# Optimization experiments

Hardware: AMD Instinct MI355X
Metric: run time of the kernel (lower is better)

Reference implementation:

```python
import jax, jax.numpy as jnp
import numpy as np

Q_DIM, KV_DIM, N_HEAD, C, OUT_DIM, N_AXIS = 256, 256, 8, 32, 256, 1
B, S = 1, 2048

def setup_inputs() -> dict:
    key = jax.random.key(0)
    ks = jax.random.split(key, 9)
    sd = 0.05
    return {
        "q_inputs": jax.random.normal(ks[0], (B, S, Q_DIM), jnp.float32),
        "kv_inputs": jax.random.normal(ks[1], (B, S, KV_DIM), jnp.float32),
        "bias": jax.random.normal(ks[2], (B, N_HEAD, S, S), jnp.float32),
        "qg_weights": jax.random.normal(ks[3], (Q_DIM, N_AXIS, N_HEAD, 2 * C), jnp.float32) * sd,
        "kv_weights": jax.random.normal(ks[4], (KV_DIM, N_AXIS, N_HEAD, 2 * C), jnp.float32) * sd,
        "qg_bias": jax.random.normal(ks[5], (N_AXIS, N_HEAD, 1, 2 * C), jnp.float32) * sd,
        "kv_bias": jax.random.normal(ks[6], (N_AXIS, N_HEAD, 1, 2 * C), jnp.float32) * sd,
        "o_weights": jax.random.normal(ks[7], (N_AXIS, N_HEAD, C, OUT_DIM), jnp.float32) * sd,
        "o_bias": jax.random.normal(ks[8], (OUT_DIM, N_AXIS), jnp.float32) * sd,
    }

def reference(q_inputs, kv_inputs, bias, qg_weights, kv_weights, qg_bias, kv_bias, o_weights, o_bias):
    scale = C ** (-0.5)
    # to_unsqueeze path: add axis dim r (=n_axis=1)
    qi = q_inputs[..., None]          # (B, q, q_dim, r)
    ki = kv_inputs[..., None]         # (B, k, kv_dim, r)
    b = bias[:, None]                 # (B, 1, h, q, k) broadcasts over r
    # per-axis, per-head QKV projections with bias
    qg = jnp.einsum('bqar,arhc->brhqc', qi, qg_weights) + qg_bias
    q, g = jnp.split(qg, 2, axis=-1)  # (B, r, h, q, c) each
    kv = jnp.einsum('bkar,arhc->brhkc', ki, kv_weights) + kv_bias
    k, v = jnp.split(kv, 2, axis=-1)  # (B, r, h, k, c) each
    logits = jnp.einsum('brhqc,brhkc->brhqk', q * scale, k) + b
    attn = jax.nn.softmax(logits, axis=-1)
    attn_out = jnp.einsum('brhqk,brhkc->brhqc', attn, v)
    attn_out = attn_out * jax.nn.sigmoid(g)  # gating
    output = jnp.einsum('brhqc,rhco->bqor', attn_out, o_weights) + o_bias
    return output[..., 0]  # squeeze the n_axis dim (to_unsqueeze path)
```

## Files before the change

kernel.cpp:

```cpp
#include <hip/hip_runtime.h>
#include <hip/hip_bf16.h>
#include <math.h>

#define SEQ   2048
#define NHEAD 8

typedef __attribute__((ext_vector_type(8))) short bf16x8;
typedef __attribute__((ext_vector_type(4))) short bf16x4;
typedef __attribute__((ext_vector_type(4))) float f32x4;

static __device__ __forceinline__ short f2bf(float f) {
    __hip_bfloat16 h = __float2bfloat16(f);
    return *reinterpret_cast<short*>(&h);
}

__global__ __launch_bounds__(256)
void prep_w_kernel(const float* __restrict__ qg_w, const float* __restrict__ kv_w,
                   const float* __restrict__ o_w, short* __restrict__ wqgT,
                   short* __restrict__ wkvT, short* __restrict__ owT)
{
    __shared__ float t[64][65];
    int bid = blockIdx.x;
    const float* src; short* dst; int N, tr, tc;
    if (bid < 32)      { src = qg_w; dst = wqgT; N = 512; tr = bid >> 3; tc = bid & 7; }
    else if (bid < 64) { bid -= 32; src = kv_w; dst = wkvT; N = 512; tr = bid >> 3; tc = bid & 7; }
    else               { bid -= 64; src = o_w;  dst = owT;  N = 256; tr = bid >> 2; tc = bid & 3; }

    const int tid = threadIdx.x;
    const int rr = tid >> 6;
    const int cc = tid & 63;
#pragma unroll
    for (int s = 0; s < 16; s++)
        t[(s << 2) + rr][cc] =
            src[(size_t)((tr << 6) + (s << 2) + rr) * N + (tc << 6) + cc];
    __syncthreads();
#pragma unroll
    for (int s = 0; s < 16; s++)
        dst[(size_t)((tc << 6) + (s << 2) + rr) * 256 + (tr << 6) + cc]
            = f2bf(t[cc][(s << 2) + rr]);
}

__global__ __launch_bounds__(256, 4)
void proj_qgkv_kernel(const float* __restrict__ q_in, const float* __restrict__ kv_in,
                      const short* __restrict__ wqgT, const short* __restrict__ wkvT,
                      const float* __restrict__ qg_b, const float* __restrict__ kv_b,
                      short* __restrict__ qs, float* __restrict__ gs,
                      short* __restrict__ ks, short* __restrict__ vP)
{
    const int z = blockIdx.z;
    const float* __restrict__ A  = z ? kv_in : q_in;
    const short* __restrict__ W  = z ? wkvT : wqgT;
    const float* __restrict__ bv = z ? kv_b : qg_b;

    const int tid = threadIdx.x;
    const int wq = tid >> 6, lane = tid & 63;
    const int ln = lane & 15, quad = lane >> 4;
    const int m0 = blockIdx.x << 6;
    const int n0 = blockIdx.y << 5;

    f32x4 acc[2];
#pragma unroll
    for (int nt = 0; nt < 2; nt++) {
        const float b = bv[n0 + (nt << 4) + ln];
        acc[nt] = (f32x4){b, b, b, b};
    }

    const float* ap = A + (size_t)(m0 + (wq << 4) + ln) * 256 + (quad << 3);
    const short* wp = W + (size_t)(n0 + ln) * 256 + (quad << 3);

    float4 a4[2][2]; bf16x8 wb[2][2];
    auto ldp = [&](int b, int k8) {
        a4[b][0] = *(const float4*)(ap + (k8 << 5));
        a4[b][1] = *(const float4*)(ap + (k8 << 5) + 4);
        wb[b][0] = *(const bf16x8*)(wp + (k8 << 5));
        wb[b][1] = *(const bf16x8*)(wp + 4096 + (k8 << 5));
    };
    ldp(0, 0);
#pragma unroll
    for (int k8 = 0; k8 < 8; k8++) {
        const int b = k8 & 1;
        if (k8 < 7) ldp(b ^ 1, k8 + 1);
        bf16x8 a;
        a[0] = f2bf(a4[b][0].x); a[1] = f2bf(a4[b][0].y);
        a[2] = f2bf(a4[b][0].z); a[3] = f2bf(a4[b][0].w);
        a[4] = f2bf(a4[b][1].x); a[5] = f2bf(a4[b][1].y);
        a[6] = f2bf(a4[b][1].z); a[7] = f2bf(a4[b][1].w);
        acc[0] = __builtin_amdgcn_mfma_f32_16x16x32_bf16(a, wb[b][0], acc[0], 0, 0, 0);
        acc[1] = __builtin_amdgcn_mfma_f32_16x16x32_bf16(a, wb[b][1], acc[1], 0, 0, 0);
    }

    const float scale = 0.17677669529663689f;
#pragma unroll
    for (int nt = 0; nt < 2; nt++) {
        const int n = n0 + (nt << 4) + ln;
        const int h = n >> 6, c2 = n & 63;
        if (z == 0) {
#pragma unroll
            for (int r = 0; r < 4; r++) {
                const int m = m0 + (wq << 4) + (quad << 2) + r;
                const float v = acc[nt][r];
                if (c2 < 32) qs[(((h << 11) + m) << 5) + c2] = f2bf(v * scale);
                else gs[(((h << 11) + m) << 5) + (c2 - 32)] = 1.0f / (1.0f + __expf(-v));
            }
        } else if (c2 < 32) {
#pragma unroll
            for (int r = 0; r < 4; r++) {
                const int m = m0 + (wq << 4) + (quad << 2) + r;
                ks[(((h << 11) + m) << 5) + c2] = f2bf(acc[nt][r]);
            }
        } else {
            const int c  = c2 - 32;
            const int kt = m0 >> 6;
            const int kc = wq >> 1;
            const int jb = (wq & 1) << 2;
            bf16x4 v4;
            v4[0] = f2bf(acc[nt][0]); v4[1] = f2bf(acc[nt][1]);
            v4[2] = f2bf(acc[nt][2]); v4[3] = f2bf(acc[nt][3]);
            *(bf16x4*)(vP + (size_t)((((h << 5) + kt) * 2 + kc) * 4 + quad) * 256
                          + (c << 3) + jb) = v4;
        }
    }
}

template<int NTILE>
__global__ __launch_bounds__(256, 3)
void attn_kernel(const short* __restrict__ qs, const short* __restrict__ ks,
                 const short* __restrict__ vP, const float* __restrict__ bias,
                 float* __restrict__ Opart, float* __restrict__ mpart,
                 float* __restrict__ lpart)
{
    const int h = blockIdx.y, z = blockIdx.z;
    const int q0 = blockIdx.x << 6;
    const int tid = threadIdx.x;
    const int wq = tid >> 6, lane = tid & 63;
    const int ln = lane & 15, quad = lane >> 4;

    const int qrow = q0 + (wq << 4) + ln;
    const bf16x8 qf = *(const bf16x8*)(qs + (((size_t)(h << 11) + qrow) << 5) + (quad << 3));

    const float L2E = 1.44269504088896f;
    float ml2 = -1e30f, l = 0.f;
    f32x4 O0 = {0, 0, 0, 0}, O1 = {0, 0, 0, 0};

    const int kbeg = z * (NTILE << 6);
    const float* bp  = bias + ((size_t)h * SEQ + qrow) * SEQ + kbeg + (quad << 2);
    const short* kp  = ks + (((size_t)(h << 11) + kbeg + ln) << 5) + (quad << 3);
    const short* vp0 = vP + (size_t)((((h << 5) + (kbeg >> 6)) * 2) * 4 + quad) * 256
                          + (ln << 3);

    f32x4 cb[2][4]; bf16x8 kf[2][4]; bf16x8 vf[2][2][2];
    auto ld = [&](int b, int t) {
#pragma unroll
        for (int mt = 0; mt < 4; mt++) {
            cb[b][mt] = *(const f32x4*)(bp + (t << 6) + (mt << 4));
            kf[b][mt] = *(const bf16x8*)(kp + ((size_t)((t << 6) + (mt << 4)) << 5));
        }
#pragma unroll
        for (int kc = 0; kc < 2; kc++)
#pragma unroll
            for (int cm = 0; cm < 2; cm++)
                vf[b][cm][kc] = *(const bf16x8*)(vp0 + (size_t)(t << 11)
                                                 + (kc << 10) + (cm << 7));
    };

    ld(0, 0);
#pragma unroll
    for (int kt = 0; kt < NTILE; kt++) {
        const int b = kt & 1;
        if (kt + 1 < NTILE) ld(b ^ 1, kt + 1);

        f32x4 S[4];
#pragma unroll
        for (int mt = 0; mt < 4; mt++)
            S[mt] = __builtin_amdgcn_mfma_f32_16x16x32_bf16(kf[b][mt], qf,
                                                            cb[b][mt], 0, 0, 0);

        float smax = S[0][0];
#pragma unroll
        for (int mt = 0; mt < 4; mt++)
#pragma unroll
            for (int r = 0; r < 4; r++) smax = fmaxf(smax, S[mt][r]);
        smax = fmaxf(smax, __shfl_xor(smax, 16));
        smax = fmaxf(smax, __shfl_xor(smax, 32));
        const float mnew = fmaxf(ml2, smax * L2E);
        const float alpha = exp2f(ml2 - mnew);
        ml2 = mnew;

        float pr[4][4];
        float rs = 0.f;
#pragma unroll
        for (int mt = 0; mt < 4; mt++)
#pragma unroll
            for (int r = 0; r < 4; r++) {
                const float p = exp2f(fmaf(S[mt][r], L2E, -mnew));
                pr[mt][r] = p;
                rs += p;
            }
        rs += __shfl_xor(rs, 16);
        rs += __shfl_xor(rs, 32);
        l = l * alpha + rs;

        short pb[4][4];
#pragma unroll
        for (int mt = 0; mt < 4; mt++)
#pragma unroll
            for (int r = 0; r < 4; r++) pb[mt][r] = f2bf(pr[mt][r]);
        bf16x8 P0 = {pb[0][0], pb[0][1], pb[0][2], pb[0][3],
                     pb[1][0], pb[1][1], pb[1][2], pb[1][3]};
        bf16x8 P1 = {pb[2][0], pb[2][1], pb[2][2], pb[2][3],
                     pb[3][0], pb[3][1], pb[3][2], pb[3][3]};

        O0 *= alpha;
        O1 *= alpha;
        O0 = __builtin_amdgcn_mfma_f32_16x16x32_bf16(vf[b][0][0], P0, O0, 0, 0, 0);
        O1 = __builtin_amdgcn_mfma_f32_16x16x32_bf16(vf[b][1][0], P0, O1, 0, 0, 0);
        O0 = __builtin_amdgcn_mfma_f32_16x16x32_bf16(vf[b][0][1], P1, O0, 0, 0, 0);
        O1 = __builtin_amdgcn_mfma_f32_16x16x32_bf16(vf[b][1][1], P1, O1, 0, 0, 0);
    }

    const size_t pb_ = (((size_t)(z * NHEAD + h)) << 11) + qrow;
    if (quad == 0) { mpart[pb_] = ml2; lpart[pb_] = l; }
    float* op = Opart + (pb_ << 5);
    *(f32x4*)(op + (quad << 2))      = O0;
    *(f32x4*)(op + 16 + (quad << 2)) = O1;
}

__global__ __launch_bounds__(256)
void combine_kernel(const float* __restrict__ Opart, const float* __restrict__ mpart,
                    const float* __restrict__ lpart, const float* __restrict__ gs,
                    short* __restrict__ att, int nsplit)
{
    const int g  = blockIdx.x * 256 + threadIdx.x;
    const int c4 = g & 7;
    const int q  = (g >> 3) & (SEQ - 1);
    const int h  = g >> 14;

    float M = -1e30f;
    for (int s = 0; s < nsplit; s++)
        M = fmaxf(M, mpart[(((size_t)s * NHEAD + h) << 11) + q]);

    float l = 0.f;
    float4 O = {0.f, 0.f, 0.f, 0.f};
    for (int s = 0; s < nsplit; s++) {
        const size_t base = (((size_t)s * NHEAD + h) << 11) + q;
        const float w = exp2f(mpart[base] - M);
        l += w * lpart[base];
        float4 o4 = *(const float4*)(Opart + (base << 5) + (c4 << 2));
        O.x = fmaf(w, o4.x, O.x); O.y = fmaf(w, o4.y, O.y);
        O.z = fmaf(w, o4.z, O.z); O.w = fmaf(w, o4.w, O.w);
    }
    const float inv = 1.0f / l;
    float4 g4 = *(const float4*)(gs + ((((size_t)h << 11) + q) << 5) + (c4 << 2));
    bf16x4 r;
    r[0] = f2bf(O.x * inv * g4.x); r[1] = f2bf(O.y * inv * g4.y);
    r[2] = f2bf(O.z * inv * g4.z); r[3] = f2bf(O.w * inv * g4.w);
    *(bf16x4*)(att + ((size_t)q << 8) + (h << 5) + (c4 << 2)) = r;
}

__global__ __launch_bounds__(256, 4)
void proj_o_kernel(const short* __restrict__ att, const short* __restrict__ owT,
                   const float* __restrict__ o_b, float* __restrict__ out)
{
    const int tid = threadIdx.x;
    const int wq = tid >> 6, lane = tid & 63;
    const int ln = lane & 15, quad = lane >> 4;
    const int m0 = blockIdx.x << 6;
    const int n0 = blockIdx.y << 4;

    const int n = n0 + ln;
    const float b = o_b[n];
    f32x4 acc = (f32x4){b, b, b, b};

    const short* ap = att + (size_t)(m0 + (wq << 4) + ln) * 256 + (quad << 3);
    const short* bp = owT + (size_t)n * 256 + (quad << 3);

    bf16x8 a2[2], w2[2];
    a2[0] = *(const bf16x8*)(ap);  w2[0] = *(const bf16x8*)(bp);
#pragma unroll
    for (int k8 = 0; k8 < 8; k8++) {
        const int b_ = k8 & 1;
        if (k8 < 7) {
            a2[b_ ^ 1] = *(const bf16x8*)(ap + ((k8 + 1) << 5));
            w2[b_ ^ 1] = *(const bf16x8*)(bp + ((k8 + 1) << 5));
        }
        acc = __builtin_amdgcn_mfma_f32_16x16x32_bf16(a2[b_], w2[b_], acc, 0, 0, 0);
    }
#pragma unroll
    for (int r = 0; r < 4; r++) {
        const int m = m0 + (wq << 4) + (quad << 2) + r;
        out[(size_t)m * 256 + n] = acc[r];
    }
}

extern "C" void kernel_launch(void* const* d_in, const int* in_sizes, int n_in,
                              void* d_out, int out_size, void* d_ws, size_t ws_size,
                              hipStream_t stream)
{
    const float* q_in  = (const float*)d_in[0];
    const float* kv_in = (const float*)d_in[1];
    const float* bias  = (const float*)d_in[2];
    const float* qg_w  = (const float*)d_in[3];
    const float* kv_w  = (const float*)d_in[4];
    const float* qg_b  = (const float*)d_in[5];
    const float* kv_b  = (const float*)d_in[6];
    const float* o_w   = (const float*)d_in[7];
    const float* o_b   = (const float*)d_in[8];
    float* out = (float*)d_out;

    char* p = (char*)d_ws;
    short* qs   = (short*)p; p += 1048576;
    short* ksb  = (short*)p; p += 1048576;
    short* vPb  = (short*)p; p += 1048576;
    short* attb = (short*)p; p += 1048576;
    short* wqgT = (short*)p; p += 262144;
    short* wkvT = (short*)p; p += 262144;
    short* owT  = (short*)p; p += 131072;
    float* gs   = (float*)p; p += 2097152;

    const size_t fixed = (size_t)(p - (char*)d_ws);
    int nsplit = 1;
    {
        const int cand[4] = {8, 4, 2, 1};
        for (int i = 0; i < 4; i++) {
            size_t ns = (size_t)cand[i];
            if (fixed + ns * (size_t)(2097152 + 2 * 65536) <= ws_size) {
                nsplit = cand[i]; break;
            }
        }
    }
    float* mp = (float*)p;
    float* lp = mp + (size_t)nsplit * NHEAD * SEQ;
    float* Op = lp + (size_t)nsplit * NHEAD * SEQ;

    hipLaunchKernelGGL(prep_w_kernel, dim3(80), dim3(256), 0, stream,
                       qg_w, kv_w, o_w, wqgT, wkvT, owT);
    hipLaunchKernelGGL(proj_qgkv_kernel, dim3(32, 16, 2), dim3(256), 0, stream,
                       q_in, kv_in, wqgT, wkvT, qg_b, kv_b, qs, gs, ksb, vPb);
    switch (nsplit) {
    case 8:
        hipLaunchKernelGGL((attn_kernel<4>), dim3(32, NHEAD, 8), dim3(256), 0, stream,
                           qs, ksb, vPb, bias, Op, mp, lp); break;
    case 4:
        hipLaunchKernelGGL((attn_kernel<8>), dim3(32, NHEAD, 4), dim3(256), 0, stream,
                           qs, ksb, vPb, bias, Op, mp, lp); break;
    case 2:
        hipLaunchKernelGGL((attn_kernel<16>), dim3(32, NHEAD, 2), dim3(256), 0, stream,
                           qs, ksb, vPb, bias, Op, mp, lp); break;
    default:
        hipLaunchKernelGGL((attn_kernel<32>), dim3(32, NHEAD, 1), dim3(256), 0, stream,
                           qs, ksb, vPb, bias, Op, mp, lp); break;
    }
    hipLaunchKernelGGL(combine_kernel, dim3(512), dim3(256), 0, stream,
                       Op, mp, lp, gs, attb, nsplit);
    hipLaunchKernelGGL(proj_o_kernel, dim3(32, 16), dim3(256), 0, stream,
                       attb, owT, o_b, out);
}
```

Baseline: 248.5 us.

## Raise attention occupancy, shrink V prefetch, and drop split-8 path

Attention now targets four blocks per SIMD instead of three. V fragments are loaded at the start of each tile instead of being double-buffered, and the probability buffer reuses the S registers, all to lower register pressure. The key-sequence split drops from 8 to at most 4, so each block handles 8 tiles, which halves the partial buffers the combine step reads. The cost is V load latency exposed inside each iteration and fewer blocks in the grid.

```diff
diff --git a/kernel.cpp b/kernel.cpp
--- a/kernel.cpp
+++ b/kernel.cpp
@@ -123,7 +123,7 @@
 }
 
 template<int NTILE>
-__global__ __launch_bounds__(256, 3)
+__global__ __launch_bounds__(256, 4)
 void attn_kernel(const short* __restrict__ qs, const short* __restrict__ ks,
                  const short* __restrict__ vP, const float* __restrict__ bias,
                  float* __restrict__ Opart, float* __restrict__ mpart,
@@ -148,26 +148,28 @@
     const short* vp0 = vP + (size_t)((((h << 5) + (kbeg >> 6)) * 2) * 4 + quad) * 256
                           + (ln << 3);
 
-    f32x4 cb[2][4]; bf16x8 kf[2][4]; bf16x8 vf[2][2][2];
-    auto ld = [&](int b, int t) {
+    f32x4 cb[2][4]; bf16x8 kf[2][4];
+    auto ld_cbkf = [&](int b, int t) {
 #pragma unroll
         for (int mt = 0; mt < 4; mt++) {
             cb[b][mt] = *(const f32x4*)(bp + (t << 6) + (mt << 4));
             kf[b][mt] = *(const bf16x8*)(kp + ((size_t)((t << 6) + (mt << 4)) << 5));
         }
-#pragma unroll
-        for (int kc = 0; kc < 2; kc++)
-#pragma unroll
-            for (int cm = 0; cm < 2; cm++)
-                vf[b][cm][kc] = *(const bf16x8*)(vp0 + (size_t)(t << 11)
-                                                 + (kc << 10) + (cm << 7));
     };
 
-    ld(0, 0);
+    ld_cbkf(0, 0);
 #pragma unroll
     for (int kt = 0; kt < NTILE; kt++) {
         const int b = kt & 1;
-        if (kt + 1 < NTILE) ld(b ^ 1, kt + 1);
+
+        bf16x8 vf[2][2];
+#pragma unroll
+        for (int kc = 0; kc < 2; kc++)
+#pragma unroll
+            for (int cm = 0; cm < 2; cm++)
+                vf[cm][kc] = *(const bf16x8*)(vp0 + (size_t)(kt << 11)
+                                              + (kc << 10) + (cm << 7));
+        if (kt + 1 < NTILE) ld_cbkf(b ^ 1, kt + 1);
 
         f32x4 S[4];
 #pragma unroll
@@ -186,36 +188,34 @@
         const float alpha = exp2f(ml2 - mnew);
         ml2 = mnew;
 
-        float pr[4][4];
         float rs = 0.f;
 #pragma unroll
         for (int mt = 0; mt < 4; mt++)
 #pragma unroll
             for (int r = 0; r < 4; r++) {
                 const float p = exp2f(fmaf(S[mt][r], L2E, -mnew));
-                pr[mt][r] = p;
+                S[mt][r] = p;
                 rs += p;
             }
         rs += __shfl_xor(rs, 16);
         rs += __shfl_xor(rs, 32);
         l = l * alpha + rs;
 
-        short pb[4][4];
-#pragma unroll
-        for (int mt = 0; mt < 4; mt++)
-#pragma unroll
-            for (int r = 0; r < 4; r++) pb[mt][r] = f2bf(pr[mt][r]);
-        bf16x8 P0 = {pb[0][0], pb[0][1], pb[0][2], pb[0][3],
-                     pb[1][0], pb[1][1], pb[1][2], pb[1][3]};
-        bf16x8 P1 = {pb[2][0], pb[2][1], pb[2][2], pb[2][3],
-                     pb[3][0], pb[3][1], pb[3][2], pb[3][3]};
+        bf16x8 P0, P1;
+#pragma unroll
+        for (int r = 0; r < 4; r++) {
+            P0[r]     = f2bf(S[0][r]);
+            P0[4 + r] = f2bf(S[1][r]);
+            P1[r]     = f2bf(S[2][r]);
+            P1[4 + r] = f2bf(S[3][r]);
+        }
 
         O0 *= alpha;
         O1 *= alpha;
-        O0 = __builtin_amdgcn_mfma_f32_16x16x32_bf16(vf[b][0][0], P0, O0, 0, 0, 0);
-        O1 = __builtin_amdgcn_mfma_f32_16x16x32_bf16(vf[b][1][0], P0, O1, 0, 0, 0);
-        O0 = __builtin_amdgcn_mfma_f32_16x16x32_bf16(vf[b][0][1], P1, O0, 0, 0, 0);
-        O1 = __builtin_amdgcn_mfma_f32_16x16x32_bf16(vf[b][1][1], P1, O1, 0, 0, 0);
+        O0 = __builtin_amdgcn_mfma_f32_16x16x32_bf16(vf[0][0], P0, O0, 0, 0, 0);
+        O1 = __builtin_amdgcn_mfma_f32_16x16x32_bf16(vf[1][0], P0, O1, 0, 0, 0);
+        O0 = __builtin_amdgcn_mfma_f32_16x16x32_bf16(vf[0][1], P1, O0, 0, 0, 0);
+        O1 = __builtin_amdgcn_mfma_f32_16x16x32_bf16(vf[1][1], P1, O1, 0, 0, 0);
     }
 
     const size_t pb_ = (((size_t)(z * NHEAD + h)) << 11) + qrow;
@@ -320,8 +320,8 @@
     const size_t fixed = (size_t)(p - (char*)d_ws);
     int nsplit = 1;
     {
-        const int cand[4] = {8, 4, 2, 1};
-        for (int i = 0; i < 4; i++) {
+        const int cand[3] = {4, 2, 1};
+        for (int i = 0; i < 3; i++) {
             size_t ns = (size_t)cand[i];
             if (fixed + ns * (size_t)(2097152 + 2 * 65536) <= ws_size) {
                 nsplit = cand[i]; break;
@@ -337,9 +337,6 @@
     hipLaunchKernelGGL(proj_qgkv_kernel, dim3(32, 16, 2), dim3(256), 0, stream,
                        q_in, kv_in, wqgT, wkvT, qg_b, kv_b, qs, gs, ksb, vPb);
     switch (nsplit) {
-    case 8:
-        hipLaunchKernelGGL((attn_kernel<4>), dim3(32, NHEAD, 8), dim3(256), 0, stream,
-                           qs, ksb, vPb, bias, Op, mp, lp); break;
     case 4:
         hipLaunchKernelGGL((attn_kernel<8>), dim3(32, NHEAD, 4), dim3(256), 0, stream,
                            qs, ksb, vPb, bias, Op, mp, lp); break;
```

New measurement: 241.8 us. 1.03x faster.
